# Performance work log

Hardware: AMD Instinct MI355X
Metric: run time of the kernel (lower is better)

## Reference

```python
import jax, jax.numpy as jnp
import numpy as np

B, N, C, H = 8, 2048, 1024, 16
D = C // H
FOCUSING_FACTOR = 3
KERNEL = 5
EPS_BN = 1e-5


def setup_inputs() -> dict:
    key = jax.random.key(0)
    ks = jax.random.split(key, 6)
    s = lambda k, shape: jax.random.normal(k, shape, dtype=jnp.float32) * 0.02
    return {
        "hidden_states": jax.random.normal(ks[0], (B, N, C), dtype=jnp.float32),
        "bn_gamma": jnp.ones((C,), jnp.float32),
        "bn_beta": jnp.zeros((C,), jnp.float32),
        "W_qkv": s(ks[1], (C, 3 * C)),
        "b_qkv": jnp.zeros((3 * C,), jnp.float32),
        "scale_p": jnp.zeros((1, 1, C), jnp.float32),
        "dwc_w": s(ks[2], (C, 1, KERNEL)),
        "dwc_b": jnp.zeros((C,), jnp.float32),
        "W_proj": s(ks[3], (C, C)),
        "b_proj": jnp.zeros((C,), jnp.float32),
    }


def _focus(t, scale):
    # Focused feature map: relu kernel, scale, then power-3 sharpening with norm restoration
    t = jax.nn.relu(t) + 1e-6
    t = t / scale
    nrm = jnp.linalg.norm(t, axis=-1, keepdims=True)
    t = t ** FOCUSING_FACTOR
    return t / jnp.linalg.norm(t, axis=-1, keepdims=True) * nrm


def reference(hidden_states, bn_gamma, bn_beta, W_qkv, b_qkv, scale_p, dwc_w, dwc_b, W_proj, b_proj):
    x = hidden_states  # (B, N, C)
    # BatchNorm1d in training mode: per-channel stats over batch and sequence
    mean = jnp.mean(x, axis=(0, 1))
    var = jnp.mean((x - mean) ** 2, axis=(0, 1))  # biased, as torch BN uses
    xn = (x - mean) * jax.lax.rsqrt(var + EPS_BN) * bn_gamma + bn_beta

    qkv = xn @ W_qkv + b_qkv
    q, k, v = jnp.split(qkv, 3, axis=-1)
    scale = jax.nn.softplus(scale_p)
    q = _focus(q, scale)
    k = _focus(k, scale)

    heads = lambda t: t.reshape(B, N, H, D).transpose(0, 2, 1, 3)  # (B,H,N,D)
    qh, kh, vh = heads(q), heads(k), heads(v)

    # Linear attention: O(N*D^2) instead of O(N^2*D)
    z = 1.0 / (jnp.einsum('bhnd,bhd->bhn', qh, kh.sum(axis=2)) + 1e-6)
    kv = jnp.einsum('bhnd,bhne->bhde', kh, vh)  # (B,H,D,D)
    o = jnp.einsum('bhnd,bhde->bhne', qh, kv) * z[..., None]
    o = o.transpose(0, 2, 1, 3).reshape(B, N, C)

    # Depthwise conv residual on v over the sequence dim
    vc = v.transpose(0, 2, 1)  # (B,C,N)
    dwc = jax.lax.conv_general_dilated(
        vc, dwc_w, window_strides=(1,), padding=[(KERNEL // 2, KERNEL // 2)],
        dimension_numbers=('NCH', 'OIH', 'NCH'), feature_group_count=C)
    dwc = (dwc + dwc_b[None, :, None]).transpose(0, 2, 1)

    return (o + dwc) @ W_proj + b_proj
```

## Files before the change

### kernel.cpp

```cpp
#include <hip/hip_runtime.h>


#define DEV __device__ __forceinline__

typedef __attribute__((ext_vector_type(8))) short bf16x8;
typedef __attribute__((ext_vector_type(4))) float f32x4;
typedef unsigned short us;

DEV float bf2f(us u) {
  union { unsigned int i; float f; } v; v.i = ((unsigned int)u) << 16; return v.f;
}
DEV us f2bf(float f) {
  union { float f; unsigned int i; } v; v.f = f;
  unsigned int r = v.i + 0x7FFFu + ((v.i >> 16) & 1u);
  return (us)(r >> 16);
}
DEV void glds16(const us* g, us* l) {
  __builtin_amdgcn_global_load_lds((const __attribute__((address_space(1))) unsigned int*)g,
                                   (__attribute__((address_space(3))) unsigned int*)l, 16, 0, 0);
}

#define MEMFENCE asm volatile("" ::: "memory")
#define BAR do { MEMFENCE; __builtin_amdgcn_s_barrier(); MEMFENCE; } while (0)
#define LGKM0 asm volatile("s_waitcnt lgkmcnt(0)" ::: "memory")

__global__ void zero_f32(float* p, int n) {
  int i = blockIdx.x * 256 + threadIdx.x;
  if (i < n) p[i] = 0.f;
}

__global__ __launch_bounds__(256) void bn_stats(const float* __restrict__ x,
                                                float* __restrict__ s_sum, float* __restrict__ s_sq) {
  int t = threadIdx.x;
  int c0 = t * 4;
  size_t row0 = (size_t)blockIdx.x * 64;
  float s[4] = {0.f,0.f,0.f,0.f}, q[4] = {0.f,0.f,0.f,0.f};
  for (int r = 0; r < 64; ++r) {
    f32x4 v = *(const f32x4*)&x[(row0 + r) * 1024 + c0];
    #pragma unroll
    for (int i = 0; i < 4; ++i) { float f = v[i]; s[i] += f; q[i] += f * f; }
  }
  #pragma unroll
  for (int i = 0; i < 4; ++i) { atomicAdd(&s_sum[c0 + i], s[i]); atomicAdd(&s_sq[c0 + i], q[i]); }
}

__global__ void bn_finalize(const float* __restrict__ s_sum, const float* __restrict__ s_sq,
                            const float* __restrict__ gamma, const float* __restrict__ beta,
                            const float* __restrict__ scalep,
                            float* __restrict__ bn_a, float* __restrict__ bn_b, float* __restrict__ invs) {
  int c = threadIdx.x;
  float mean = s_sum[c] * (1.0f / 16384.0f);
  float var  = s_sq[c] * (1.0f / 16384.0f) - mean * mean;
  float a = gamma[c] * rsqrtf(var + 1e-5f);
  bn_a[c] = a;
  bn_b[c] = beta[c] - mean * a;
  float sv = scalep[c];
  float sp = (sv > 20.f) ? sv : log1pf(expf(sv));
  invs[c] = 1.0f / sp;
}

__global__ __launch_bounds__(256) void xn_to_bf16(const float* __restrict__ x,
                                                  const float* __restrict__ bn_a, const float* __restrict__ bn_b,
                                                  us* __restrict__ xn) {
  size_t base = ((size_t)blockIdx.x * 256 + threadIdx.x) * 8;
  int c = (int)(base & 1023);
  f32x4 a0 = *(const f32x4*)&x[base];
  f32x4 a1 = *(const f32x4*)&x[base + 4];
  uint4 o; us* uo = (us*)&o;
  #pragma unroll
  for (int i = 0; i < 4; ++i) uo[i] = f2bf(bn_a[c + i] * a0[i] + bn_b[c + i]);
  #pragma unroll
  for (int i = 0; i < 4; ++i) uo[4 + i] = f2bf(bn_a[c + 4 + i] * a1[i] + bn_b[c + 4 + i]);
  *(uint4*)&xn[base] = o;
}

__global__ __launch_bounds__(256) void transpose_f32_bf16(const float* __restrict__ in,
                                                          us* __restrict__ out, int R, int Cc) {
  __shared__ float tile[64 * 65];
  int tx = blockIdx.x * 64, ty = blockIdx.y * 64;
  int t = threadIdx.x;
  {
    int rr = t >> 4, g = t & 15;
    #pragma unroll
    for (int p = 0; p < 4; ++p) {
      int r = p * 16 + rr;
      f32x4 v = *(const f32x4*)&in[(size_t)(ty + r) * Cc + tx + g * 4];
      #pragma unroll
      for (int i = 0; i < 4; ++i) tile[r * 65 + g * 4 + i] = v[i];
    }
  }
  __syncthreads();
  {
    int rr = t >> 3, g = t & 7;
    #pragma unroll
    for (int p = 0; p < 2; ++p) {
      int nl = p * 32 + rr;
      uint4 v; us* u = (us*)&v;
      #pragma unroll
      for (int j = 0; j < 8; ++j) u[j] = f2bf(tile[(g * 8 + j) * 65 + nl]);
      *(uint4*)&out[(size_t)(tx + nl) * R + ty + g * 8] = v;
    }
  }
}

template <typename OutT>
__global__ __launch_bounds__(512, 2) void gemm256(const us* __restrict__ A,
                                                  const us* __restrict__ Bt,
                                                  const float* __restrict__ bias,
                                                  OutT* __restrict__ Ca,
                                                  OutT* __restrict__ Cb) {
  constexpr int GK = 1024;
  __shared__ __align__(16) us As[2][2][128 * 64];
  __shared__ __align__(16) us Bs[2][2][128 * 64];
  int t = threadIdx.x;
  int wid = t >> 6, lane = t & 63;
  int l16 = lane & 15, qd = lane >> 4;
  int nwx = gridDim.x;
  int id = blockIdx.y * nwx + blockIdx.x;
  int nwg = nwx * (int)gridDim.y;
  int sw = (id & 7) * (nwg >> 3) + (id >> 3);
  int n0 = (sw % nwx) * 256, m0 = (sw / nwx) * 256;

  int rr = lane >> 3, lg = (lane & 7) ^ rr;
  const us* Asrc = A + (size_t)(m0 + wid * 8 + rr) * GK + lg * 8;
  const us* Bsrc = Bt + (size_t)(n0 + wid * 8 + rr) * GK + lg * 8;

  int wr = wid >> 2, wc = wid & 3;
  int bh = wc >> 1, brow0 = (wc & 1) * 64;

  f32x4 acc[8][4];
  const f32x4 zero4 = {0.f, 0.f, 0.f, 0.f};
  #pragma unroll
  for (int i = 0; i < 8; ++i)
    #pragma unroll
    for (int j = 0; j < 4; ++j) acc[i][j] = zero4;

  auto STAGE_A = [&](int kt, int b) {
    const us* src = Asrc + kt * 64;
    us* dst = (us*)&As[b][0][0] + wid * 512;
    #pragma unroll
    for (int g = 0; g < 4; ++g)
      glds16(src + (size_t)(g * 64) * GK, dst + g * 4096);
  };
  auto STAGE_B = [&](int kt, int b) {
    const us* src = Bsrc + kt * 64;
    us* dst = (us*)&Bs[b][0][0] + wid * 512;
    #pragma unroll
    for (int g = 0; g < 4; ++g)
      glds16(src + (size_t)(g * 64) * GK, dst + g * 4096);
  };
  auto LDA = [&](bf16x8* dst, int i0, int ks, int b) {
    #pragma unroll
    for (int i = 0; i < 4; ++i) {
      int r = (i0 + i) * 16 + l16;
      int sl = (ks * 4 + qd) ^ (r & 7);
      dst[i] = *(const bf16x8*)&As[b][wr][r * 64 + sl * 8];
    }
  };
  auto LDB = [&](bf16x8* dst, int ks, int b) {
    #pragma unroll
    for (int j = 0; j < 4; ++j) {
      int r = brow0 + j * 16 + l16;
      int sl = (ks * 4 + qd) ^ (r & 7);
      dst[j] = *(const bf16x8*)&Bs[b][bh][r * 64 + sl * 8];
    }
  };
  auto MM = [&](int i0, bf16x8* a4, bf16x8* b4) {
    __builtin_amdgcn_s_setprio(1);
    #pragma unroll
    for (int i = 0; i < 4; ++i)
      #pragma unroll
      for (int j = 0; j < 4; ++j)
        acc[i0 + i][j] = __builtin_amdgcn_mfma_f32_16x16x32_bf16(a4[i], b4[j], acc[i0 + i][j], 0, 0, 0);
    __builtin_amdgcn_s_setprio(0);
  };

  STAGE_A(0, 0); STAGE_B(0, 0);
  asm volatile("s_waitcnt vmcnt(0)" ::: "memory");
  BAR;

  for (int kt = 0; kt < 16; ++kt) {
    int buf = kt & 1, nxt = buf ^ 1;
    bf16x8 afl[4], afh[4], bfv[4];
    LDA(afl, 0, 0, buf); LDB(bfv, 0, buf);
    if (kt < 15) STAGE_A(kt + 1, nxt);
    BAR; LGKM0; MM(0, afl, bfv); BAR;
    LDA(afh, 4, 0, buf);
    if (kt < 15) STAGE_B(kt + 1, nxt);
    BAR; LGKM0; MM(4, afh, bfv); BAR;
    LDA(afl, 0, 1, buf); LDB(bfv, 1, buf);
    BAR; LGKM0; MM(0, afl, bfv); BAR;
    LDA(afh, 4, 1, buf);
    asm volatile("s_waitcnt vmcnt(0)" ::: "memory");
    BAR; LGKM0; MM(4, afh, bfv); BAR;
  }

  OutT* Cp; int col0;
  if (n0 < 1024) { Cp = Ca; col0 = n0; } else { Cp = Cb; col0 = n0 - 1024; }
  #pragma unroll
  for (int i = 0; i < 8; ++i) {
    int row = m0 + wr * 128 + i * 16 + qd * 4;
    #pragma unroll
    for (int j = 0; j < 4; ++j) {
      int fc = n0 + wc * 64 + j * 16 + l16;
      float bv = bias[fc];
      int col = col0 + wc * 64 + j * 16 + l16;
      #pragma unroll
      for (int r = 0; r < 4; ++r) {
        float val = acc[i][j][r] + bv;
        if constexpr (sizeof(OutT) == 2)
          ((us*)Cp)[(size_t)(row + r) * 1024 + col] = f2bf(val);
        else
          ((float*)Cp)[(size_t)(row + r) * 1024 + col] = val;
      }
    }
  }
}

__global__ __launch_bounds__(256) void focus_kernel(us* __restrict__ buf,
                                                    const float* __restrict__ invs) {
  int row = blockIdx.x;
  us* p = buf + (size_t)row * 1024;
  int t = threadIdx.x;
  int c0 = t * 4;
  uint2 v = *(uint2*)&p[c0];
  us* u = (us*)&v;
  float ti[4]; float s2 = 0.f, s6 = 0.f;
  #pragma unroll
  for (int i = 0; i < 4; ++i) {
    float f = bf2f(u[i]);
    f = fmaxf(f, 0.f) + 1e-6f;
    f *= invs[c0 + i];
    ti[i] = f;
    float f2 = f * f;
    s2 += f2; s6 += f2 * f2 * f2;
  }
  #pragma unroll
  for (int off = 32; off > 0; off >>= 1) { s2 += __shfl_down(s2, off); s6 += __shfl_down(s6, off); }
  __shared__ float red[8]; __shared__ float bc;
  int wid = t >> 6, lane = t & 63;
  if (lane == 0) { red[wid] = s2; red[4 + wid] = s6; }
  __syncthreads();
  if (t == 0) {
    float a = red[0] + red[1] + red[2] + red[3];
    float b2 = red[4] + red[5] + red[6] + red[7];
    bc = sqrtf(a / b2);
  }
  __syncthreads();
  float factor = bc;
  #pragma unroll
  for (int i = 0; i < 4; ++i) u[i] = f2bf(ti[i] * ti[i] * ti[i] * factor);
  *(uint2*)&p[c0] = v;
}

__global__ __launch_bounds__(256) void attn_stats3(const us* __restrict__ kbuf,
                                                   const us* __restrict__ vbuf,
                                                   float* __restrict__ ksum,
                                                   float* __restrict__ kvpart) {
  int cx = blockIdx.x, h = blockIdx.y, b = blockIdx.z, bh = b * 16 + h;
  int t = threadIdx.x, wid = t >> 6, lane = t & 63;
  int l16 = lane & 15, qd = lane >> 4;
  int wm = (wid & 1) * 32, wn = (wid >> 1) * 32;
  __shared__ __align__(16) us kT[64 * 80];
  __shared__ __align__(16) us vT[64 * 80];
  const f32x4 zero4 = {0.f, 0.f, 0.f, 0.f};
  f32x4 acc[2][2];
  #pragma unroll
  for (int i = 0; i < 2; ++i)
    #pragma unroll
    for (int j = 0; j < 2; ++j) acc[i][j] = zero4;
  float ksacc = 0.f;
  int np = (t & 31) * 2, ch0 = (t >> 5) * 8;

  for (int ck = 0; ck < 4; ++ck) {
    __syncthreads();
    size_t base = ((size_t)b * 2048 + cx * 256 + ck * 64 + np) * 1024 + h * 64 + ch0;
    uint4 k0 = *(const uint4*)&kbuf[base];
    uint4 k1 = *(const uint4*)&kbuf[base + 1024];
    uint4 v0 = *(const uint4*)&vbuf[base];
    uint4 v1 = *(const uint4*)&vbuf[base + 1024];
    us* pk0 = (us*)&k0; us* pk1 = (us*)&k1; us* pv0 = (us*)&v0; us* pv1 = (us*)&v1;
    #pragma unroll
    for (int i = 0; i < 8; ++i) {
      unsigned int pk = (unsigned int)pk0[i] | ((unsigned int)pk1[i] << 16);
      unsigned int pv = (unsigned int)pv0[i] | ((unsigned int)pv1[i] << 16);
      *(unsigned int*)&kT[(ch0 + i) * 80 + np] = pk;
      *(unsigned int*)&vT[(ch0 + i) * 80 + np] = pv;
    }
    __syncthreads();
    if (t < 64) {
      #pragma unroll
      for (int g = 0; g < 8; ++g) {
        bf16x8 kk = *(const bf16x8*)&kT[t * 80 + g * 8];
        #pragma unroll
        for (int j = 0; j < 8; ++j) ksacc += bf2f(((us*)&kk)[j]);
      }
    }
    #pragma unroll
    for (int ks = 0; ks < 2; ++ks) {
      bf16x8 af[2], bfr[2];
      #pragma unroll
      for (int i = 0; i < 2; ++i) {
        af[i]  = *(const bf16x8*)&kT[(wm + i * 16 + l16) * 80 + ks * 32 + qd * 8];
        bfr[i] = *(const bf16x8*)&vT[(wn + i * 16 + l16) * 80 + ks * 32 + qd * 8];
      }
      #pragma unroll
      for (int i = 0; i < 2; ++i)
        #pragma unroll
        for (int j = 0; j < 2; ++j)
          acc[i][j] = __builtin_amdgcn_mfma_f32_16x16x32_bf16(af[i], bfr[j], acc[i][j], 0, 0, 0);
    }
  }
  float* pp = kvpart + ((size_t)cx * 128 + bh) * 4096;
  #pragma unroll
  for (int i = 0; i < 2; ++i) {
    int d = wm + i * 16 + qd * 4;
    #pragma unroll
    for (int j = 0; j < 2; ++j) {
      int e = wn + j * 16 + l16;
      #pragma unroll
      for (int r = 0; r < 4; ++r) pp[(d + r) * 64 + e] = acc[i][j][r];
    }
  }
  if (t < 64) atomicAdd(&ksum[bh * 64 + t], ksacc);
}

__global__ __launch_bounds__(256) void kv_reduce(const float* __restrict__ part, us* __restrict__ kvT) {
  int bh = blockIdx.x;
  int t = threadIdx.x;
  __shared__ float kvl[4096];
  #pragma unroll
  for (int p = 0; p < 16; ++p) {
    int i = p * 256 + t;
    float s = 0.f;
    #pragma unroll
    for (int c = 0; c < 8; ++c) s += part[((size_t)c * 128 + bh) * 4096 + i];
    kvl[i] = s;
  }
  __syncthreads();
  #pragma unroll
  for (int p = 0; p < 2; ++p) {
    int idx = p * 256 + t;
    int e = idx >> 3, d0 = (idx & 7) * 8;
    uint4 o; us* uo = (us*)&o;
    #pragma unroll
    for (int i = 0; i < 8; ++i) uo[i] = f2bf(kvl[(d0 + i) * 64 + e]);
    *(uint4*)&kvT[(size_t)bh * 4096 + e * 64 + d0] = o;
  }
}

__global__ __launch_bounds__(256) void attn_o2(us* __restrict__ qod,
                                               const us* __restrict__ vbuf,
                                               const float* __restrict__ ksum,
                                               const us* __restrict__ kvT,
                                               const float* __restrict__ dwcw,
                                               const float* __restrict__ dwcb) {
  int nt = blockIdx.x, h = blockIdx.y, b = blockIdx.z, bh = b * 16 + h;
  int t = threadIdx.x, wid = t >> 6, lane = t & 63;
  int l16 = lane & 15, qd = lane >> 4;
  __shared__ __align__(16) us qs[128 * 64];
  __shared__ __align__(16) us bs[64 * 64];
  __shared__ __align__(16) us vs[132 * 64];
  __shared__ float zl[128];
  __shared__ float ksl[64];
  __shared__ float wl[64 * 5];
  __shared__ float bl[64];
  int rS = t >> 3, gS = t & 7;
  size_t qbase = ((size_t)b * 2048 + nt * 128) * 1024 + h * 64;
  #pragma unroll
  for (int p = 0; p < 4; ++p) {
    int r = p * 32 + rS;
    uint4 v = *(const uint4*)&qod[qbase + (size_t)r * 1024 + gS * 8];
    *(uint4*)&qs[r * 64 + ((gS ^ (r & 7)) * 8)] = v;
  }
  #pragma unroll
  for (int p = 0; p < 2; ++p) {
    int r = p * 32 + rS;
    uint4 v = *(const uint4*)&kvT[(size_t)bh * 4096 + r * 64 + gS * 8];
    *(uint4*)&bs[r * 64 + ((gS ^ (r & 7)) * 8)] = v;
  }
  int n0 = nt * 128;
  #pragma unroll
  for (int p = 0; p < 5; ++p) {
    int idx = p * 256 + t;
    if (idx < 1056) {
      int r = idx >> 3, g = idx & 7;
      int n = n0 - 2 + r;
      uint4 v = make_uint4(0, 0, 0, 0);
      if (n >= 0 && n < 2048)
        v = *(const uint4*)&vbuf[((size_t)b * 2048 + n) * 1024 + h * 64 + g * 8];
      *(uint4*)&vs[r * 64 + g * 8] = v;
    }
  }
  if (t < 64) {
    ksl[t] = ksum[bh * 64 + t];
    bl[t] = dwcb[h * 64 + t];
    #pragma unroll
    for (int j = 0; j < 5; ++j) wl[t * 5 + j] = dwcw[(h * 64 + t) * 5 + j];
  }
  __syncthreads();
  if (t < 128) {
    float zs = 0.f;
    #pragma unroll
    for (int g = 0; g < 8; ++g) {
      bf16x8 qv = *(const bf16x8*)&qs[t * 64 + ((g ^ (t & 7)) * 8)];
      #pragma unroll
      for (int j = 0; j < 8; ++j) zs += bf2f(((us*)&qv)[j]) * ksl[g * 8 + j];
    }
    zl[t] = 1.f / (zs + 1e-6f);
  }
  __syncthreads();
  const f32x4 zero4 = {0.f, 0.f, 0.f, 0.f};
  f32x4 acc[2][4];
  #pragma unroll
  for (int i = 0; i < 2; ++i)
    #pragma unroll
    for (int j = 0; j < 4; ++j) acc[i][j] = zero4;
  #pragma unroll
  for (int ks = 0; ks < 2; ++ks) {
    bf16x8 af[2], bfr[4];
    #pragma unroll
    for (int i = 0; i < 2; ++i) {
      int ml = (wid * 2 + i) * 16 + l16;
      af[i] = *(const bf16x8*)&qs[ml * 64 + (((ks * 4 + qd) ^ (ml & 7)) * 8)];
    }
    #pragma unroll
    for (int j = 0; j < 4; ++j) {
      int nl = j * 16 + l16;
      bfr[j] = *(const bf16x8*)&bs[nl * 64 + (((ks * 4 + qd) ^ (nl & 7)) * 8)];
    }
    #pragma unroll
    for (int i = 0; i < 2; ++i)
      #pragma unroll
      for (int j = 0; j < 4; ++j)
        acc[i][j] = __builtin_amdgcn_mfma_f32_16x16x32_bf16(af[i], bfr[j], acc[i][j], 0, 0, 0);
  }
  #pragma unroll
  for (int i = 0; i < 2; ++i) {
    int rl0 = (wid * 2 + i) * 16 + qd * 4;
    #pragma unroll
    for (int j = 0; j < 4; ++j) {
      int e = j * 16 + l16;
      float w0 = wl[e * 5], w1 = wl[e * 5 + 1], w2 = wl[e * 5 + 2], w3 = wl[e * 5 + 3], w4 = wl[e * 5 + 4];
      float vv[8];
      #pragma unroll
      for (int m = 0; m < 8; ++m) vv[m] = bf2f(vs[(rl0 + m) * 64 + e]);
      float bb = bl[e];
      #pragma unroll
      for (int r = 0; r < 4; ++r) {
        float dwc = vv[r] * w0 + vv[r + 1] * w1 + vv[r + 2] * w2 + vv[r + 3] * w3 + vv[r + 4] * w4;
        float o = acc[i][j][r] * zl[rl0 + r] + dwc + bb;
        qod[qbase + (size_t)(rl0 + r) * 1024 + e] = f2bf(o);
      }
    }
  }
}

extern "C" void kernel_launch(void* const* d_in, const int* in_sizes, int n_in,
                              void* d_out, int out_size, void* d_ws, size_t ws_size,
                              hipStream_t stream) {
  const float* x      = (const float*)d_in[0];
  const float* gamma  = (const float*)d_in[1];
  const float* beta   = (const float*)d_in[2];
  const float* Wqkv   = (const float*)d_in[3];
  const float* bqkv   = (const float*)d_in[4];
  const float* scalep = (const float*)d_in[5];
  const float* dwcw   = (const float*)d_in[6];
  const float* dwcb   = (const float*)d_in[7];
  const float* Wproj  = (const float*)d_in[8];
  const float* bproj  = (const float*)d_in[9];
  float* out = (float*)d_out;

  float* wsf = (float*)d_ws;
  float* s_sum  = wsf;
  float* s_sq   = wsf + 1024;
  float* ksum   = wsf + 2048;
  float* bn_a   = wsf + 10240;
  float* bn_b   = wsf + 11264;
  float* invs   = wsf + 12288;
  float* kvpart = wsf + 13312;
  us* kvT = (us*)(wsf + 4207616);
  us* wtq = (us*)(wsf + 4469760);
  us* wtp = (us*)(wsf + 6042624);
  us* kq  = (us*)(wsf + 6566912);
  us* vbf = (us*)d_out;
  us* xnb = (us*)d_out + 16777216;

  zero_f32<<<40, 256, 0, stream>>>(wsf, 10240);
  bn_stats<<<256, 256, 0, stream>>>(x, s_sum, s_sq);
  bn_finalize<<<1, 1024, 0, stream>>>(s_sum, s_sq, gamma, beta, scalep, bn_a, bn_b, invs);
  xn_to_bf16<<<8192, 256, 0, stream>>>(x, bn_a, bn_b, xnb);
  transpose_f32_bf16<<<dim3(48, 16), 256, 0, stream>>>(Wqkv, wtq, 1024, 3072);
  transpose_f32_bf16<<<dim3(16, 16), 256, 0, stream>>>(Wproj, wtp, 1024, 1024);

  gemm256<us><<<dim3(8, 64), 512, 0, stream>>>(xnb, wtq + 1024 * 1024, bqkv + 1024, kq, vbf);
  focus_kernel<<<16384, 256, 0, stream>>>(kq, invs);
  attn_stats3<<<dim3(8, 16, 8), 256, 0, stream>>>(kq, vbf, ksum, kvpart);
  kv_reduce<<<128, 256, 0, stream>>>(kvpart, kvT);
  gemm256<us><<<dim3(4, 64), 512, 0, stream>>>(xnb, wtq, bqkv, kq, kq);
  focus_kernel<<<16384, 256, 0, stream>>>(kq, invs);
  attn_o2<<<dim3(16, 16, 8), 256, 0, stream>>>(kq, vbf, ksum, kvT, dwcw, dwcb);
  gemm256<float><<<dim3(4, 64), 512, 0, stream>>>(kq, wtp, bproj, out, out);
}
```

Before: 397.1 us.

## Deepen GEMM LDS pipeline to four stages with K=32 sub-tiles

Restructures the 256x256 bf16 GEMM mainloop from a double-buffered K=64 pipeline into a 4-deep ring of K=32 tiles, prefetching three tiles ahead with partial vmcnt waits instead of draining to zero every iteration. The LDS layout is repacked so each buffer holds both row halves side by side, and the swizzle and fragment addressing are adjusted to match. The aim is to hide more global-load latency and cut barriers per unit of MFMA work. In exchange, the prologue and epilogue handling is more intricate and the vmcnt accounting must be exact.

```diff
diff --git a/kernel.cpp b/kernel.cpp
--- a/kernel.cpp
+++ b/kernel.cpp
@@ -110,8 +110,8 @@
                                                   OutT* __restrict__ Ca,
                                                   OutT* __restrict__ Cb) {
   constexpr int GK = 1024;
-  __shared__ __align__(16) us As[2][2][128 * 64];
-  __shared__ __align__(16) us Bs[2][2][128 * 64];
+  __shared__ __align__(16) us As[4][128 * 64];
+  __shared__ __align__(16) us Bs[4][128 * 64];
   int t = threadIdx.x;
   int wid = t >> 6, lane = t & 63;
   int l16 = lane & 15, qd = lane >> 4;
@@ -121,12 +121,13 @@
   int sw = (id & 7) * (nwg >> 3) + (id >> 3);
   int n0 = (sw % nwx) * 256, m0 = (sw / nwx) * 256;
 
-  int rr = lane >> 3, lg = (lane & 7) ^ rr;
-  const us* Asrc = A + (size_t)(m0 + wid * 8 + rr) * GK + lg * 8;
-  const us* Bsrc = Bt + (size_t)(n0 + wid * 8 + rr) * GK + lg * 8;
+  int rr = lane >> 3, sl = lane & 7;
+  int lg = sl ^ rr;
+  int grp = lg >> 2, ch = lg & 3;
+  const us* Asrc = A + (size_t)(m0 + wid * 8 + rr + 128 * grp) * GK + ch * 8;
+  const us* Bsrc = Bt + (size_t)(n0 + wid * 8 + rr + 128 * grp) * GK + ch * 8;
 
   int wr = wid >> 2, wc = wid & 3;
-  int bh = wc >> 1, brow0 = (wc & 1) * 64;
 
   f32x4 acc[8][4];
   const f32x4 zero4 = {0.f, 0.f, 0.f, 0.f};
@@ -135,34 +136,35 @@
     #pragma unroll
     for (int j = 0; j < 4; ++j) acc[i][j] = zero4;
 
-  auto STAGE_A = [&](int kt, int b) {
-    const us* src = Asrc + kt * 64;
-    us* dst = (us*)&As[b][0][0] + wid * 512;
-    #pragma unroll
-    for (int g = 0; g < 4; ++g)
-      glds16(src + (size_t)(g * 64) * GK, dst + g * 4096);
+  auto STAGE_A = [&](int kt) {
+    int b = kt & 3;
+    const us* src = Asrc + (size_t)kt * 32;
+    us* dst = (us*)&As[0][0] + b * 8192 + (wid * 8) * 64;
+    glds16(src, dst);
+    glds16(src + (size_t)64 * GK, dst + 64 * 64);
   };
-  auto STAGE_B = [&](int kt, int b) {
-    const us* src = Bsrc + kt * 64;
-    us* dst = (us*)&Bs[b][0][0] + wid * 512;
-    #pragma unroll
-    for (int g = 0; g < 4; ++g)
-      glds16(src + (size_t)(g * 64) * GK, dst + g * 4096);
+  auto STAGE_B = [&](int kt) {
+    int b = kt & 3;
+    const us* src = Bsrc + (size_t)kt * 32;
+    us* dst = (us*)&Bs[0][0] + b * 8192 + (wid * 8) * 64;
+    glds16(src, dst);
+    glds16(src + (size_t)64 * GK, dst + 64 * 64);
   };
-  auto LDA = [&](bf16x8* dst, int i0, int ks, int b) {
+  auto LDA = [&](bf16x8* d4, int i0, int b) {
     #pragma unroll
     for (int i = 0; i < 4; ++i) {
       int r = (i0 + i) * 16 + l16;
-      int sl = (ks * 4 + qd) ^ (r & 7);
-      dst[i] = *(const bf16x8*)&As[b][wr][r * 64 + sl * 8];
+      int ps = (wr * 4 + qd) ^ (r & 7);
+      d4[i] = *(const bf16x8*)((const us*)&As[0][0] + b * 8192 + r * 64 + ps * 8);
     }
   };
-  auto LDB = [&](bf16x8* dst, int ks, int b) {
+  auto LDB = [&](bf16x8* d4, int b) {
     #pragma unroll
     for (int j = 0; j < 4; ++j) {
-      int r = brow0 + j * 16 + l16;
-      int sl = (ks * 4 + qd) ^ (r & 7);
-      dst[j] = *(const bf16x8*)&Bs[b][bh][r * 64 + sl * 8];
+      int rowb = wc * 64 + j * 16 + l16;
+      int grpb = rowb >> 7, rb = rowb & 127;
+      int ps = (grpb * 4 + qd) ^ (rb & 7);
+      d4[j] = *(const bf16x8*)((const us*)&Bs[0][0] + b * 8192 + rb * 64 + ps * 8);
     }
   };
   auto MM = [&](int i0, bf16x8* a4, bf16x8* b4) {
@@ -175,25 +177,31 @@
     __builtin_amdgcn_s_setprio(0);
   };
 
-  STAGE_A(0, 0); STAGE_B(0, 0);
-  asm volatile("s_waitcnt vmcnt(0)" ::: "memory");
+  auto TILE = [&](int kt, bool stage, int vm) {
+    int buf = kt & 3;
+    bf16x8 afl[4], afh[4], bfv[4];
+    LDA(afl, 0, buf); LDB(bfv, buf);
+    if (stage) STAGE_A(kt + 3);
+    BAR; LGKM0; MM(0, afl, bfv); BAR;
+    LDA(afh, 4, buf);
+    if (stage) STAGE_B(kt + 3);
+    BAR; LGKM0; MM(4, afh, bfv);
+    if (vm == 8)      asm volatile("s_waitcnt vmcnt(8)" ::: "memory");
+    else if (vm == 4) asm volatile("s_waitcnt vmcnt(4)" ::: "memory");
+    else if (vm == 0) asm volatile("s_waitcnt vmcnt(0)" ::: "memory");
+    BAR;
+  };
+
+  STAGE_A(-3 + 3); STAGE_B(0);
+  STAGE_A(1 - 3 + 3); STAGE_B(1);
+  STAGE_A(2); STAGE_B(2);
+  asm volatile("s_waitcnt vmcnt(8)" ::: "memory");
   BAR;
 
-  for (int kt = 0; kt < 16; ++kt) {
-    int buf = kt & 1, nxt = buf ^ 1;
-    bf16x8 afl[4], afh[4], bfv[4];
-    LDA(afl, 0, 0, buf); LDB(bfv, 0, buf);
-    if (kt < 15) STAGE_A(kt + 1, nxt);
-    BAR; LGKM0; MM(0, afl, bfv); BAR;
-    LDA(afh, 4, 0, buf);
-    if (kt < 15) STAGE_B(kt + 1, nxt);
-    BAR; LGKM0; MM(4, afh, bfv); BAR;
-    LDA(afl, 0, 1, buf); LDB(bfv, 1, buf);
-    BAR; LGKM0; MM(0, afl, bfv); BAR;
-    LDA(afh, 4, 1, buf);
-    asm volatile("s_waitcnt vmcnt(0)" ::: "memory");
-    BAR; LGKM0; MM(4, afh, bfv); BAR;
-  }
+  for (int kt = 0; kt < 29; ++kt) TILE(kt, true, 8);
+  TILE(29, false, 4);
+  TILE(30, false, 0);
+  TILE(31, false, -1);
 
   OutT* Cp; int col0;
   if (n0 < 1024) { Cp = Ca; col0 = n0; } else { Cp = Cb; col0 = n0 - 1024; }
```

New measurement: 435.4 us. 1.1x slower.
